# Kernel optimization log

Hardware: AMD Instinct MI355X
Metric: run time of the kernel (lower is better)

The kernel has to match this reference:

```python
import jax, jax.numpy as jnp
import numpy as np

N_NODES = 50000
N_EDGES = 800000


def _norm(deg):
    # DGL: norm = deg^-0.5 with inf (zero-degree) replaced by 0
    return jnp.where(deg > 0, jax.lax.rsqrt(jnp.maximum(deg, 1.0)), 0.0)


def setup_inputs() -> dict:
    key = jax.random.key(0)
    ks = jax.random.split(key, 8)
    x = jax.random.normal(ks[0], (N_NODES, 128), dtype=jnp.float32)
    W1 = jax.random.normal(ks[1], (128, 128), dtype=jnp.float32) * (1.0 / np.sqrt(128))
    b1 = jnp.zeros((128,), dtype=jnp.float32)
    W2 = jax.random.normal(ks[2], (128, 8), dtype=jnp.float32) * (1.0 / np.sqrt(128))
    b2 = jnp.zeros((8,), dtype=jnp.float32)
    src = jax.random.randint(ks[3], (N_EDGES,), 0, N_NODES, dtype=jnp.int32)
    dst = jax.random.randint(ks[4], (N_EDGES,), 0, N_NODES, dtype=jnp.int32)
    graph_ids = jnp.sort(jax.random.randint(ks[5], (N_NODES,), 0, 100, dtype=jnp.int32))
    return {"x": x, "W1": W1, "b1": b1, "W2": W2, "b2": b2,
            "src": src, "dst": dst, "graph_ids": graph_ids, "num_graphs": 100}


def _graph_conv(x, W, b, src, dst, norm_src, norm_dst):
    # GraphConv norm='both': out = D_in^{-1/2} A (D_out^{-1/2} x W) + b
    h = x @ W                                   # [N, F_out]
    msg = h[src] * norm_src[src, None]          # gather + src norm, [E, F_out]
    agg = jax.ops.segment_sum(msg, dst, num_segments=x.shape[0])  # scatter-add
    return agg * norm_dst[:, None] + b


def reference(x, W1, b1, W2, b2, src, dst, graph_ids, num_graphs):
    n = x.shape[0]
    ones_e = jnp.ones((src.shape[0],), dtype=x.dtype)
    deg_out = jax.ops.segment_sum(ones_e, src, num_segments=n)
    deg_in = jax.ops.segment_sum(ones_e, dst, num_segments=n)
    norm_src = _norm(deg_out)
    norm_dst = _norm(deg_in)

    h = _graph_conv(x, W1, b1, src, dst, norm_src, norm_dst)
    h = jax.nn.relu(h)
    h = _graph_conv(h, W2, b2, src, dst, norm_src, norm_dst)

    # dgl.mean_nodes: per-graph mean of node features
    counts = jax.ops.segment_sum(jnp.ones((n,), dtype=x.dtype), graph_ids,
                                 num_segments=num_graphs)
    sums = jax.ops.segment_sum(h, graph_ids, num_segments=num_graphs)
    return sums / jnp.maximum(counts, 1.0)[:, None]
```

## Files before the change

### kernel.cpp

```cpp
#include <hip/hip_runtime.h>

#define F1 128
#define F2 8
#define CAP 64
#define RH 8192
#define ECH 16384
#define BK 32

typedef unsigned short us8 __attribute__((ext_vector_type(8)));

__device__ inline unsigned short f2bf(float f) {
  unsigned u = __float_as_uint(f);
  u += 0x7FFF + ((u >> 16) & 1);
  return (unsigned short)(u >> 16);
}
__device__ inline float bf2f(unsigned short h) {
  return __uint_as_float(((unsigned)h) << 16);
}

__global__ void k_pack(const int* __restrict__ src, const int* __restrict__ dst,
                       unsigned short* __restrict__ src16, unsigned short* __restrict__ dst16,
                       int E, int Epad) {
  int e = blockIdx.x * 256 + threadIdx.x;
  if (e < Epad) {
    src16[e] = (e < E) ? (unsigned short)src[e] : (unsigned short)0xFFFF;
    dst16[e] = (e < E) ? (unsigned short)dst[e] : (unsigned short)0xFFFF;
  }
}

__global__ __launch_bounds__(256) void k_hist(const unsigned short* __restrict__ src16,
                                              const unsigned short* __restrict__ dst16,
                                              int* __restrict__ partialA,
                                              int* __restrict__ partialB,
                                              int Epad, int N) {
  __shared__ int binsA[RH];
  __shared__ int binsB[RH];
  int range0 = blockIdx.x * RH;
  int c = blockIdx.y;
  int t = threadIdx.x;
  for (int i = t; i < RH; i += 256) { binsA[i] = 0; binsB[i] = 0; }
  __syncthreads();
  int e0 = c * ECH, e1 = min(e0 + ECH, Epad);
  for (int base = e0 + t * 8; base < e1; base += 2048) {
    us8 a = *(const us8*)&src16[base];
    us8 b = *(const us8*)&dst16[base];
#pragma unroll
    for (int j = 0; j < 8; ++j) {
      int sn = (int)a[j] - range0;
      if ((unsigned)sn < (unsigned)RH) atomicAdd(&binsA[sn], 1);
      int dn = (int)b[j] - range0;
      if ((unsigned)dn < (unsigned)RH) atomicAdd(&binsB[dn], 1);
    }
  }
  __syncthreads();
  for (int i = t; i < RH; i += 256) {
    int n = range0 + i;
    if (n < N) {
      partialA[c * N + n] = binsA[i];
      partialB[c * N + n] = binsB[i];
    }
  }
}

__global__ void k_starts(const int* __restrict__ partialA, const int* __restrict__ partialB,
                         int* __restrict__ starts, int* __restrict__ cnt,
                         float* __restrict__ norm_src, float* __restrict__ norm_dst,
                         unsigned short* __restrict__ esrc16,
                         unsigned short* __restrict__ h1n,
                         int N, int NCH) {
  int n = blockIdx.x * 256 + threadIdx.x;
  if (n < 16) {
    us8 z = {0, 0, 0, 0, 0, 0, 0, 0};
    *(us8*)&h1n[(size_t)N * 128 + n * 8] = z;
  }
  if (n < N) {
    int dout = 0;
    for (int c = 0; c < NCH; ++c) dout += partialA[c * N + n];
    int run = n * CAP;
    for (int c = 0; c < NCH; ++c) {
      starts[c * N + n] = run;
      run += partialB[c * N + n];
    }
    int din = run - n * CAP;
    int cn = min(din, CAP);
    cnt[n] = cn;
    int cp = (cn + 15) & ~15;
    for (int pos = cn; pos < cp; ++pos) esrc16[n * CAP + pos] = (unsigned short)N;
    norm_src[n] = dout > 0 ? rsqrtf((float)dout) : 0.f;
    norm_dst[n] = din > 0 ? rsqrtf((float)din) : 0.f;
  }
}

__global__ __launch_bounds__(256) void k_scatter(const unsigned short* __restrict__ src16,
                                                 const unsigned short* __restrict__ dst16,
                                                 const int* __restrict__ starts,
                                                 unsigned short* __restrict__ esrc16,
                                                 int Epad, int N) {
  __shared__ int cur[RH];
  int range0 = blockIdx.x * RH;
  int c = blockIdx.y;
  int t = threadIdx.x;
  for (int i = t; i < RH; i += 256) {
    int n = range0 + i;
    cur[i] = (n < N) ? starts[c * N + n] : 0;
  }
  __syncthreads();
  int e0 = c * ECH, e1 = min(e0 + ECH, Epad);
  for (int base = e0 + t * 8; base < e1; base += 2048) {
    us8 a = *(const us8*)&src16[base];
    us8 b = *(const us8*)&dst16[base];
#pragma unroll
    for (int j = 0; j < 8; ++j) {
      int dn = (int)b[j] - range0;
      if ((unsigned)dn < (unsigned)RH) {
        int node = range0 + dn;
        int p = atomicAdd(&cur[dn], 1);
        if (p < (node + 1) * CAP) esrc16[p] = a[j];
      }
    }
  }
}

__global__ __launch_bounds__(256) void k_gemm1(const float* __restrict__ x,
                                               const float* __restrict__ W1,
                                               const float* __restrict__ norm_src,
                                               unsigned short* __restrict__ h1n, int N) {
  __shared__ float xsT[BK][132];
  __shared__ float Wl[BK][132];
  int row0 = blockIdx.x * 128;
  int tid = threadIdx.x;
  int tc = tid & 15;
  int tr = tid >> 4;
  float acc[8][8] = {{0.f}};

  for (int kb = 0; kb < 128; kb += BK) {
    __syncthreads();
#pragma unroll
    for (int it = 0; it < 4; ++it) {
      int i = tid + it * 256;
      int r = i >> 3, kq = i & 7;
      int grow = row0 + r;
      float4 v = make_float4(0.f, 0.f, 0.f, 0.f);
      if (grow < N) v = *(const float4*)&x[(size_t)grow * 128 + kb + kq * 4];
      xsT[kq * 4 + 0][r] = v.x;
      xsT[kq * 4 + 1][r] = v.y;
      xsT[kq * 4 + 2][r] = v.z;
      xsT[kq * 4 + 3][r] = v.w;
    }
#pragma unroll
    for (int it = 0; it < 4; ++it) {
      int i = tid + it * 256;
      int k = i >> 5, c4 = i & 31;
      *(float4*)&Wl[k][c4 * 4] = *(const float4*)&W1[(size_t)(kb + k) * 128 + c4 * 4];
    }
    __syncthreads();
#pragma unroll 2
    for (int k = 0; k < BK; ++k) {
      float4 xa = *(float4*)&xsT[k][tr * 8];
      float4 xb = *(float4*)&xsT[k][tr * 8 + 4];
      float4 wa = *(float4*)&Wl[k][tc * 8];
      float4 wb = *(float4*)&Wl[k][tc * 8 + 4];
      float xs[8] = {xa.x, xa.y, xa.z, xa.w, xb.x, xb.y, xb.z, xb.w};
      float ws[8] = {wa.x, wa.y, wa.z, wa.w, wb.x, wb.y, wb.z, wb.w};
#pragma unroll
      for (int i = 0; i < 8; ++i)
#pragma unroll
        for (int j = 0; j < 8; ++j) acc[i][j] += xs[i] * ws[j];
    }
  }
#pragma unroll
  for (int i = 0; i < 8; ++i) {
    int grow = row0 + tr * 8 + i;
    if (grow < N) {
      float ns = norm_src[grow];
      us8 o;
#pragma unroll
      for (int j = 0; j < 8; ++j) o[j] = f2bf(acc[i][j] * ns);
      *(us8*)&h1n[(size_t)grow * 128 + tc * 8] = o;
    }
  }
}

__global__ __launch_bounds__(256) void k_agg1f(const unsigned short* __restrict__ h1n,
                                               const int* __restrict__ cnt,
                                               const unsigned short* __restrict__ esrc16,
                                               const float* __restrict__ norm_dst,
                                               const float* __restrict__ norm_src,
                                               const float* __restrict__ b1,
                                               const float* __restrict__ W2,
                                               float* __restrict__ h2n, int N) {
  int tid = threadIdx.x;
  int wid = (blockIdx.x * 256 + tid) >> 6;
  int lane = tid & 63;
  if (wid >= N) return;
  int q = lane >> 4;
  int fl = lane & 15;
  int cp = (cnt[wid] + 15) & ~15;
  int i0 = wid * CAP;
  int i1 = i0 + cp;
  float acc[8] = {0.f, 0.f, 0.f, 0.f, 0.f, 0.f, 0.f, 0.f};
  for (int i = i0; i < i1; i += 64) {
    int c64 = min(64, i1 - i);
    for (int t = 0; t < c64; t += 16) {
      int be = i + t + (q << 2);
      ushort4 ss = *(const ushort4*)&esrc16[be];
      us8 v0 = *(const us8*)&h1n[(size_t)ss.x * 128 + fl * 8];
      us8 v1 = *(const us8*)&h1n[(size_t)ss.y * 128 + fl * 8];
      us8 v2 = *(const us8*)&h1n[(size_t)ss.z * 128 + fl * 8];
      us8 v3 = *(const us8*)&h1n[(size_t)ss.w * 128 + fl * 8];
#pragma unroll
      for (int j = 0; j < 8; ++j)
        acc[j] += (bf2f(v0[j]) + bf2f(v1[j])) + (bf2f(v2[j]) + bf2f(v3[j]));
    }
  }
#pragma unroll
  for (int j = 0; j < 8; ++j) acc[j] += __shfl_down(acc[j], 32);
#pragma unroll
  for (int j = 0; j < 8; ++j) acc[j] += __shfl_down(acc[j], 16);
  if (lane < 16) {
    float nd = norm_dst[wid];
    float4 bb0 = *(const float4*)&b1[fl * 8];
    float4 bb1 = *(const float4*)&b1[fl * 8 + 4];
    float r[8];
    r[0] = fmaxf(acc[0] * nd + bb0.x, 0.f);
    r[1] = fmaxf(acc[1] * nd + bb0.y, 0.f);
    r[2] = fmaxf(acc[2] * nd + bb0.z, 0.f);
    r[3] = fmaxf(acc[3] * nd + bb0.w, 0.f);
    r[4] = fmaxf(acc[4] * nd + bb1.x, 0.f);
    r[5] = fmaxf(acc[5] * nd + bb1.y, 0.f);
    r[6] = fmaxf(acc[6] * nd + bb1.z, 0.f);
    r[7] = fmaxf(acc[7] * nd + bb1.w, 0.f);
    float4 pa = make_float4(0.f, 0.f, 0.f, 0.f);
    float4 pb = make_float4(0.f, 0.f, 0.f, 0.f);
#pragma unroll
    for (int jj = 0; jj < 8; ++jj) {
      float4 wa = *(const float4*)&W2[(fl * 8 + jj) * 8];
      float4 wb = *(const float4*)&W2[(fl * 8 + jj) * 8 + 4];
      pa.x += r[jj] * wa.x; pa.y += r[jj] * wa.y;
      pa.z += r[jj] * wa.z; pa.w += r[jj] * wa.w;
      pb.x += r[jj] * wb.x; pb.y += r[jj] * wb.y;
      pb.z += r[jj] * wb.z; pb.w += r[jj] * wb.w;
    }
#pragma unroll
    for (int d = 8; d >= 1; d >>= 1) {
      pa.x += __shfl_down(pa.x, d); pa.y += __shfl_down(pa.y, d);
      pa.z += __shfl_down(pa.z, d); pa.w += __shfl_down(pa.w, d);
      pb.x += __shfl_down(pb.x, d); pb.y += __shfl_down(pb.y, d);
      pb.z += __shfl_down(pb.z, d); pb.w += __shfl_down(pb.w, d);
    }
    if (lane == 0) {
      float ns = norm_src[wid];
      pa.x *= ns; pa.y *= ns; pa.z *= ns; pa.w *= ns;
      pb.x *= ns; pb.y *= ns; pb.z *= ns; pb.w *= ns;
      *(float4*)&h2n[(size_t)wid * 8] = pa;
      *(float4*)&h2n[(size_t)wid * 8 + 4] = pb;
    }
  }
}

__global__ __launch_bounds__(256) void k_agg2pool(const float* __restrict__ h2n,
                                                  const int* __restrict__ cnt,
                                                  const unsigned short* __restrict__ esrc16,
                                                  const float* __restrict__ norm_dst,
                                                  const float* __restrict__ b2,
                                                  const int* __restrict__ gids,
                                                  float* __restrict__ gsum, int N) {
  __shared__ float bins[16 * 8];
  __shared__ int sg0;
  int tid = threadIdx.x;
  if (tid < 128) bins[tid] = 0.f;
  int base = blockIdx.x * 32;
  if (tid == 0) sg0 = gids[min(base, N - 1)];
  __syncthreads();
  int node = base + (tid >> 3);
  int j = tid & 7;
  if (node < N) {
    int i0 = node * CAP;
    int i1 = i0 + cnt[node];
    float acc = 0.f;
    for (int i = i0; i < i1; i += 8) {
      int c8 = min(8, i1 - i);
      int eid = (i + j < i1) ? (int)esrc16[i + j] : 0;
      for (int t = 0; t < c8; ++t) {
        int s = __shfl(eid, t, 8);
        acc += h2n[s * 8 + j];
      }
    }
    float r = acc * norm_dst[node] + b2[j];
    int delta = gids[node] - sg0;
    if (delta < 16) atomicAdd(&bins[delta * 8 + j], r);
    else atomicAdd(&gsum[gids[node] * 8 + j], r);
  }
  __syncthreads();
  if (tid < 128) {
    float v = bins[tid];
    if (v != 0.f) atomicAdd(&gsum[(sg0 + (tid >> 3)) * 8 + (tid & 7)], v);
  }
}

__global__ void k_final(const float* __restrict__ gsum, const int* __restrict__ gids,
                        float* __restrict__ out, int NG, int N) {
  int i = blockIdx.x * 256 + threadIdx.x;
  if (i < NG * F2) {
    int g = i >> 3;
    int lo = 0, hi = N;
    while (lo < hi) { int m = (lo + hi) >> 1; if (gids[m] < g) lo = m + 1; else hi = m; }
    int lb = lo;
    lo = 0; hi = N;
    while (lo < hi) { int m = (lo + hi) >> 1; if (gids[m] <= g) lo = m + 1; else hi = m; }
    int cnt = lo - lb;
    out[i] = gsum[i] / fmaxf((float)cnt, 1.f);
  }
}

extern "C" void kernel_launch(void* const* d_in, const int* in_sizes, int n_in,
                              void* d_out, int out_size, void* d_ws, size_t ws_size,
                              hipStream_t stream) {
  const float* x  = (const float*)d_in[0];
  const float* W1 = (const float*)d_in[1];
  const float* b1 = (const float*)d_in[2];
  const float* W2 = (const float*)d_in[3];
  const float* b2 = (const float*)d_in[4];
  const int* src  = (const int*)d_in[5];
  const int* dst  = (const int*)d_in[6];
  const int* gids = (const int*)d_in[7];
  int N = in_sizes[0] / F1;
  int E = in_sizes[5];
  int NG = out_size / F2;
  float* out = (float*)d_out;

  int Epad = (E + 2047) & ~2047;
  int NR  = (N + RH - 1) / RH;
  int NCH = (Epad + ECH - 1) / ECH;

  char* p = (char*)d_ws;
  auto alloc = [&](size_t bytes) -> void* {
    void* r = (void*)p;
    p += (bytes + 255) & ~(size_t)255;
    return r;
  };
  float* gsum    = (float*)alloc((size_t)NG * F2 * 4);
  size_t zero_bytes = (size_t)((char*)p - (char*)gsum);
  unsigned short* src16 = (unsigned short*)alloc((size_t)Epad * 2);
  unsigned short* dst16 = (unsigned short*)alloc((size_t)Epad * 2);
  int* cnt       = (int*)alloc((size_t)N * 4);
  float* norm_src = (float*)alloc((size_t)N * 4);
  float* norm_dst = (float*)alloc((size_t)N * 4);
  unsigned short* esrc16 = (unsigned short*)alloc((size_t)N * CAP * 2);
  unsigned short* h1n = (unsigned short*)alloc((size_t)(N + 1) * F1 * 2);
  float* h2n     = (float*)alloc((size_t)N * F2 * 4);
  int* partialA  = (int*)alloc((size_t)NCH * N * 4);
  int* partialB  = (int*)alloc((size_t)NCH * N * 4);
  int* starts    = (int*)alloc((size_t)NCH * N * 4);
  (void)ws_size; (void)n_in;

  hipMemsetAsync(gsum, 0, zero_bytes, stream);

  k_pack<<<(Epad + 255) / 256, 256, 0, stream>>>(src, dst, src16, dst16, E, Epad);
  k_hist<<<dim3(NR, NCH), 256, 0, stream>>>(src16, dst16, partialA, partialB, Epad, N);
  k_starts<<<(N + 255) / 256, 256, 0, stream>>>(partialA, partialB, starts, cnt,
                                                norm_src, norm_dst, esrc16, h1n, N, NCH);
  k_scatter<<<dim3(NR, NCH), 256, 0, stream>>>(src16, dst16, starts, esrc16, Epad, N);
  k_gemm1<<<(N + 127) / 128, 256, 0, stream>>>(x, W1, norm_src, h1n, N);
  k_agg1f<<<(N + 3) / 4, 256, 0, stream>>>(h1n, cnt, esrc16, norm_dst, norm_src, b1, W2, h2n, N);
  k_agg2pool<<<((N * 8 + 255) / 256), 256, 0, stream>>>(h2n, cnt, esrc16, norm_dst, b2, gids, gsum, N);
  k_final<<<(NG * F2 + 255) / 256, 256, 0, stream>>>(gsum, gids, out, NG, N);
}
```

Before: 259.1 us.

## Map one node per 16 lanes in layer-1 aggregation and vectorize layer-2 gather

```diff
diff --git a/kernel.cpp b/kernel.cpp
--- a/kernel.cpp
+++ b/kernel.cpp
@@ -67,12 +67,14 @@
                          float* __restrict__ norm_src, float* __restrict__ norm_dst,
                          unsigned short* __restrict__ esrc16,
                          unsigned short* __restrict__ h1n,
+                         float* __restrict__ h2n,
                          int N, int NCH) {
   int n = blockIdx.x * 256 + threadIdx.x;
   if (n < 16) {
     us8 z = {0, 0, 0, 0, 0, 0, 0, 0};
     *(us8*)&h1n[(size_t)N * 128 + n * 8] = z;
   }
+  if (n < 8) h2n[(size_t)N * 8 + n] = 0.f;
   if (n < N) {
     int dout = 0;
     for (int c = 0; c < NCH; ++c) dout += partialA[c * N + n];
@@ -190,20 +192,18 @@
                                                const float* __restrict__ W2,
                                                float* __restrict__ h2n, int N) {
   int tid = threadIdx.x;
-  int wid = (blockIdx.x * 256 + tid) >> 6;
   int lane = tid & 63;
-  if (wid >= N) return;
-  int q = lane >> 4;
+  int g = lane >> 4;
   int fl = lane & 15;
-  int cp = (cnt[wid] + 15) & ~15;
-  int i0 = wid * CAP;
-  int i1 = i0 + cp;
+  int node = (blockIdx.x * 256 + tid - lane) / 16 + g;
+  if (node >= N) return;
+  int cp = (cnt[node] + 15) & ~15;
+  int i0 = node * CAP;
   float acc[8] = {0.f, 0.f, 0.f, 0.f, 0.f, 0.f, 0.f, 0.f};
-  for (int i = i0; i < i1; i += 64) {
-    int c64 = min(64, i1 - i);
-    for (int t = 0; t < c64; t += 16) {
-      int be = i + t + (q << 2);
-      ushort4 ss = *(const ushort4*)&esrc16[be];
+  for (int i = 0; i < cp; i += 16) {
+#pragma unroll
+    for (int t4 = 0; t4 < 16; t4 += 4) {
+      ushort4 ss = *(const ushort4*)&esrc16[i0 + i + t4];
       us8 v0 = *(const us8*)&h1n[(size_t)ss.x * 128 + fl * 8];
       us8 v1 = *(const us8*)&h1n[(size_t)ss.y * 128 + fl * 8];
       us8 v2 = *(const us8*)&h1n[(size_t)ss.z * 128 + fl * 8];
@@ -213,48 +213,42 @@
         acc[j] += (bf2f(v0[j]) + bf2f(v1[j])) + (bf2f(v2[j]) + bf2f(v3[j]));
     }
   }
-#pragma unroll
-  for (int j = 0; j < 8; ++j) acc[j] += __shfl_down(acc[j], 32);
-#pragma unroll
-  for (int j = 0; j < 8; ++j) acc[j] += __shfl_down(acc[j], 16);
-  if (lane < 16) {
-    float nd = norm_dst[wid];
-    float4 bb0 = *(const float4*)&b1[fl * 8];
-    float4 bb1 = *(const float4*)&b1[fl * 8 + 4];
-    float r[8];
-    r[0] = fmaxf(acc[0] * nd + bb0.x, 0.f);
-    r[1] = fmaxf(acc[1] * nd + bb0.y, 0.f);
-    r[2] = fmaxf(acc[2] * nd + bb0.z, 0.f);
-    r[3] = fmaxf(acc[3] * nd + bb0.w, 0.f);
-    r[4] = fmaxf(acc[4] * nd + bb1.x, 0.f);
-    r[5] = fmaxf(acc[5] * nd + bb1.y, 0.f);
-    r[6] = fmaxf(acc[6] * nd + bb1.z, 0.f);
-    r[7] = fmaxf(acc[7] * nd + bb1.w, 0.f);
-    float4 pa = make_float4(0.f, 0.f, 0.f, 0.f);
-    float4 pb = make_float4(0.f, 0.f, 0.f, 0.f);
-#pragma unroll
-    for (int jj = 0; jj < 8; ++jj) {
-      float4 wa = *(const float4*)&W2[(fl * 8 + jj) * 8];
-      float4 wb = *(const float4*)&W2[(fl * 8 + jj) * 8 + 4];
-      pa.x += r[jj] * wa.x; pa.y += r[jj] * wa.y;
-      pa.z += r[jj] * wa.z; pa.w += r[jj] * wa.w;
-      pb.x += r[jj] * wb.x; pb.y += r[jj] * wb.y;
-      pb.z += r[jj] * wb.z; pb.w += r[jj] * wb.w;
-    }
-#pragma unroll
-    for (int d = 8; d >= 1; d >>= 1) {
-      pa.x += __shfl_down(pa.x, d); pa.y += __shfl_down(pa.y, d);
-      pa.z += __shfl_down(pa.z, d); pa.w += __shfl_down(pa.w, d);
-      pb.x += __shfl_down(pb.x, d); pb.y += __shfl_down(pb.y, d);
-      pb.z += __shfl_down(pb.z, d); pb.w += __shfl_down(pb.w, d);
-    }
-    if (lane == 0) {
-      float ns = norm_src[wid];
-      pa.x *= ns; pa.y *= ns; pa.z *= ns; pa.w *= ns;
-      pb.x *= ns; pb.y *= ns; pb.z *= ns; pb.w *= ns;
-      *(float4*)&h2n[(size_t)wid * 8] = pa;
-      *(float4*)&h2n[(size_t)wid * 8 + 4] = pb;
-    }
+  float nd = norm_dst[node];
+  float4 bb0 = *(const float4*)&b1[fl * 8];
+  float4 bb1 = *(const float4*)&b1[fl * 8 + 4];
+  float r[8];
+  r[0] = fmaxf(acc[0] * nd + bb0.x, 0.f);
+  r[1] = fmaxf(acc[1] * nd + bb0.y, 0.f);
+  r[2] = fmaxf(acc[2] * nd + bb0.z, 0.f);
+  r[3] = fmaxf(acc[3] * nd + bb0.w, 0.f);
+  r[4] = fmaxf(acc[4] * nd + bb1.x, 0.f);
+  r[5] = fmaxf(acc[5] * nd + bb1.y, 0.f);
+  r[6] = fmaxf(acc[6] * nd + bb1.z, 0.f);
+  r[7] = fmaxf(acc[7] * nd + bb1.w, 0.f);
+  float4 pa = make_float4(0.f, 0.f, 0.f, 0.f);
+  float4 pb = make_float4(0.f, 0.f, 0.f, 0.f);
+#pragma unroll
+  for (int jj = 0; jj < 8; ++jj) {
+    float4 wa = *(const float4*)&W2[(fl * 8 + jj) * 8];
+    float4 wb = *(const float4*)&W2[(fl * 8 + jj) * 8 + 4];
+    pa.x += r[jj] * wa.x; pa.y += r[jj] * wa.y;
+    pa.z += r[jj] * wa.z; pa.w += r[jj] * wa.w;
+    pb.x += r[jj] * wb.x; pb.y += r[jj] * wb.y;
+    pb.z += r[jj] * wb.z; pb.w += r[jj] * wb.w;
+  }
+#pragma unroll
+  for (int d = 8; d >= 1; d >>= 1) {
+    pa.x += __shfl_down(pa.x, d); pa.y += __shfl_down(pa.y, d);
+    pa.z += __shfl_down(pa.z, d); pa.w += __shfl_down(pa.w, d);
+    pb.x += __shfl_down(pb.x, d); pb.y += __shfl_down(pb.y, d);
+    pb.z += __shfl_down(pb.z, d); pb.w += __shfl_down(pb.w, d);
+  }
+  if (fl == 0) {
+    float ns = norm_src[node];
+    pa.x *= ns; pa.y *= ns; pa.z *= ns; pa.w *= ns;
+    pb.x *= ns; pb.y *= ns; pb.z *= ns; pb.w *= ns;
+    *(float4*)&h2n[(size_t)node * 8] = pa;
+    *(float4*)&h2n[(size_t)node * 8 + 4] = pb;
   }
 }
 
@@ -275,16 +269,13 @@
   int node = base + (tid >> 3);
   int j = tid & 7;
   if (node < N) {
+    int cp = (cnt[node] + 15) & ~15;
     int i0 = node * CAP;
-    int i1 = i0 + cnt[node];
     float acc = 0.f;
-    for (int i = i0; i < i1; i += 8) {
-      int c8 = min(8, i1 - i);
-      int eid = (i + j < i1) ? (int)esrc16[i + j] : 0;
-      for (int t = 0; t < c8; ++t) {
-        int s = __shfl(eid, t, 8);
-        acc += h2n[s * 8 + j];
-      }
+    for (int i = 0; i < cp; i += 4) {
+      ushort4 ss = *(const ushort4*)&esrc16[i0 + i];
+      acc += (h2n[(size_t)ss.x * 8 + j] + h2n[(size_t)ss.y * 8 + j]) +
+             (h2n[(size_t)ss.z * 8 + j] + h2n[(size_t)ss.w * 8 + j]);
     }
     float r = acc * norm_dst[node] + b2[j];
     int delta = gids[node] - sg0;
@@ -348,7 +339,7 @@
   float* norm_dst = (float*)alloc((size_t)N * 4);
   unsigned short* esrc16 = (unsigned short*)alloc((size_t)N * CAP * 2);
   unsigned short* h1n = (unsigned short*)alloc((size_t)(N + 1) * F1 * 2);
-  float* h2n     = (float*)alloc((size_t)N * F2 * 4);
+  float* h2n     = (float*)alloc((size_t)(N + 1) * F2 * 4);
   int* partialA  = (int*)alloc((size_t)NCH * N * 4);
   int* partialB  = (int*)alloc((size_t)NCH * N * 4);
   int* starts    = (int*)alloc((size_t)NCH * N * 4);
@@ -359,10 +350,10 @@
   k_pack<<<(Epad + 255) / 256, 256, 0, stream>>>(src, dst, src16, dst16, E, Epad);
   k_hist<<<dim3(NR, NCH), 256, 0, stream>>>(src16, dst16, partialA, partialB, Epad, N);
   k_starts<<<(N + 255) / 256, 256, 0, stream>>>(partialA, partialB, starts, cnt,
-                                                norm_src, norm_dst, esrc16, h1n, N, NCH);
+                                                norm_src, norm_dst, esrc16, h1n, h2n, N, NCH);
   k_scatter<<<dim3(NR, NCH), 256, 0, stream>>>(src16, dst16, starts, esrc16, Epad, N);
   k_gemm1<<<(N + 127) / 128, 256, 0, stream>>>(x, W1, norm_src, h1n, N);
-  k_agg1f<<<(N + 3) / 4, 256, 0, stream>>>(h1n, cnt, esrc16, norm_dst, norm_src, b1, W2, h2n, N);
+  k_agg1f<<<(N + 15) / 16, 256, 0, stream>>>(h1n, cnt, esrc16, norm_dst, norm_src, b1, W2, h2n, N);
   k_agg2pool<<<((N * 8 + 255) / 256), 256, 0, stream>>>(h2n, cnt, esrc16, norm_dst, b2, gids, gsum, N);
   k_final<<<(NG * F2 + 255) / 256, 256, 0, stream>>>(gsum, gids, out, NG, N);
 }
```

After: 244.0 us. 5.8% less time.
